# Kernel tuning notes

Hardware: AMD Instinct MI355X
Metric: run time of the kernel (lower is better)

## Reference

```python
import jax, jax.numpy as jnp
import numpy as np

B, T, D, H, G = 32, 1000, 512, 512, 8
LN_EPS = 1e-5


def setup_inputs() -> dict:
    key = jax.random.key(0)
    ks = jax.random.split(key, 6)
    return {
        "x": jax.random.normal(ks[0], (B, T, D), jnp.float32),
        "w_in": jax.random.normal(ks[1], (G, D // G, H // G), jnp.float32) * 0.05,
        "w_rec_W": jax.random.normal(ks[2], (2 * H, H), jnp.float32) * 0.05,
        "u_rec": jax.random.normal(ks[3], (2 * H, H), jnp.float32) * 0.05,
        "ln_gamma": jnp.ones((2 * H,), jnp.float32),
        "ln_beta": jnp.zeros((2 * H,), jnp.float32),
        "w_out": jax.random.normal(ks[4], (G, H // G, D // G), jnp.float32) * 0.05,
    }


def grouped_linear(x, w):
    # x: [B,T,G*I], w: [G,I,Ho] -> [B,T,G*Ho]
    b, t, _ = x.shape
    g, i, ho = w.shape
    y = jnp.einsum('btgi,gih->btgh', x.reshape(b, t, g, i), w)
    return y.reshape(b, t, g * ho)


def layernorm(w, gamma, beta):
    mu = jnp.mean(w, axis=-1, keepdims=True)
    var = jnp.var(w, axis=-1, keepdims=True)
    return (w - mu) * jax.lax.rsqrt(var + LN_EPS) * gamma + beta


def ligru_scan(w, u):
    # w: [B,T,2H] precomputed input projection; u: [2H,H] recurrent weight
    ut = u.T  # [H, 2H]
    h0 = jnp.zeros((w.shape[0], u.shape[1]), w.dtype)

    def step(h, wt):
        gates = wt + h @ ut            # [B, 2H]
        at, zt = jnp.split(gates, 2, axis=1)
        zt = jax.nn.sigmoid(zt)
        hcand = jax.nn.relu(at)        # drop_mask = 1.0 (eval)
        h = zt * h + (1.0 - zt) * hcand
        return h, h

    _, hs = jax.lax.scan(step, h0, jnp.swapaxes(w, 0, 1))  # [T,B,H]
    return jnp.swapaxes(hs, 0, 1)  # [B,T,H]


def reference(x, w_in, w_rec_W, u_rec, ln_gamma, ln_beta, w_out):
    h_in = grouped_linear(x, w_in)              # [B,T,H]
    w = jnp.einsum('bth,gh->btg', h_in, w_rec_W)  # [B,T,2H]
    w = layernorm(w, ln_gamma, ln_beta)
    h = ligru_scan(w, u_rec)                    # [B,T,H]
    return grouped_linear(h, w_out)             # [B,T,D]
```

## Files before the change

kernel.cpp:

```cpp
#include <hip/hip_runtime.h>
#include <cstddef>

#define B_SZ 32
#define T_LEN 1000
#define LN_EPS 1e-5f

typedef short bf16x8 __attribute__((ext_vector_type(8)));
typedef float f32x4 __attribute__((ext_vector_type(4)));

__device__ __forceinline__ unsigned short f2bf(float f) {
    unsigned u = __builtin_bit_cast(unsigned, f);
    u += 0x7FFFu + ((u >> 16) & 1u);
    return (unsigned short)(u >> 16);
}

__global__ __launch_bounds__(256) void k1(const float* __restrict__ x,
                                          const float* __restrict__ w_in,
                                          const float* __restrict__ w_rec,
                                          unsigned short* __restrict__ hin,
                                          unsigned short* __restrict__ wrt,
                                          unsigned int* __restrict__ hbuf) {
    __shared__ alignas(16) float xt[16][512];
    const int tid  = threadIdx.x;
    const int gidx = blockIdx.x * 256 + tid;
    const int row0 = blockIdx.x * 16;

    if (gidx < 2 * 32 * 512) hbuf[gidx] = 0u;

    if (gidx < 65536) {
        int lane = gidx & 63;
        int nt   = (gidx >> 6) & 63;
        int kt   = gidx >> 12;
        int n    = nt * 16 + (lane & 15);
        int k0   = kt * 32 + (lane >> 4) * 8;
        const float* src = w_rec + (size_t)n * 512 + k0;
        unsigned short* dst = wrt + (size_t)gidx * 8;
#pragma unroll
        for (int j = 0; j < 8; ++j) dst[j] = f2bf(src[j]);
    }

    for (int i = tid; i < 16 * 128; i += 256) {
        int rr = i >> 7, c4 = i & 127;
        ((float4*)xt[rr])[c4] =
            ((const float4*)(x + (size_t)(row0 + rr) * 512))[c4];
    }
    __syncthreads();

    for (int q = 0; q < 2; ++q) {
        const int c = tid + (q << 8);
        const int g = c >> 6, o = c & 63;
        const float* wb = w_in + (g << 12) + o;
        float wcol[64];
#pragma unroll
        for (int ii = 0; ii < 64; ++ii) wcol[ii] = wb[ii << 6];
#pragma unroll 4
        for (int rr = 0; rr < 16; ++rr) {
            float acc = 0.f;
#pragma unroll
            for (int ii = 0; ii < 64; ++ii) acc += xt[rr][(g << 6) + ii] * wcol[ii];
            hin[(size_t)(row0 + rr) * 512 + c] = f2bf(acc);
        }
    }
}

#define ALD 536
__global__ __launch_bounds__(256) void k2(const unsigned short* __restrict__ hin,
                                          const unsigned short* __restrict__ wrt,
                                          const float* __restrict__ gamma,
                                          const float* __restrict__ beta,
                                          float* __restrict__ w_pre) {
    __shared__ alignas(16) unsigned short At[32 * ALD];
    __shared__ float redS[4][32];
    __shared__ float redQ[4][32];
    __shared__ float stat[2][32];

    const int tid  = threadIdx.x;
    const int w    = tid >> 6;
    const int l    = tid & 63;
    const int kgrp = l >> 4;
    const int lc   = l & 15;
    const int row0 = blockIdx.x * 32;

    for (int sidx = tid; sidx < 2048; sidx += 256) {
        int r = sidx >> 6, sg = sidx & 63;
        *(bf16x8*)(At + r * ALD + sg * 8) =
            *(const bf16x8*)(hin + (size_t)(row0 + r) * 512 + sg * 8);
    }
    __syncthreads();

    f32x4 acc[2][16];
#pragma unroll
    for (int fr = 0; fr < 2; ++fr)
#pragma unroll
        for (int n = 0; n < 16; ++n) acc[fr][n] = f32x4{0.f, 0.f, 0.f, 0.f};

    for (int kt = 0; kt < 16; ++kt) {
        bf16x8 a0 = *(const bf16x8*)(At + (lc)      * ALD + kt * 32 + kgrp * 8);
        bf16x8 a1 = *(const bf16x8*)(At + (16 + lc) * ALD + kt * 32 + kgrp * 8);
        const unsigned short* bb =
            wrt + (((size_t)kt * 64 + w * 16) * 64 + l) * 8;
#pragma unroll
        for (int ntl = 0; ntl < 16; ++ntl) {
            bf16x8 bf = *(const bf16x8*)(bb + (size_t)ntl * 512);
            acc[0][ntl] = __builtin_amdgcn_mfma_f32_16x16x32_bf16(a0, bf, acc[0][ntl], 0, 0, 0);
            acc[1][ntl] = __builtin_amdgcn_mfma_f32_16x16x32_bf16(a1, bf, acc[1][ntl], 0, 0, 0);
        }
    }

    float sums[2][4] = {{0.f}}, sqs[2][4] = {{0.f}};
#pragma unroll
    for (int fr = 0; fr < 2; ++fr)
#pragma unroll
        for (int ntl = 0; ntl < 16; ++ntl)
#pragma unroll
            for (int r = 0; r < 4; ++r) {
                float v = acc[fr][ntl][r];
                sums[fr][r] += v;
                sqs[fr][r]  += v * v;
            }
#pragma unroll
    for (int off = 1; off < 16; off <<= 1)
#pragma unroll
        for (int fr = 0; fr < 2; ++fr)
#pragma unroll
            for (int r = 0; r < 4; ++r) {
                sums[fr][r] += __shfl_xor(sums[fr][r], off);
                sqs[fr][r]  += __shfl_xor(sqs[fr][r], off);
            }
    if (lc == 0) {
#pragma unroll
        for (int fr = 0; fr < 2; ++fr)
#pragma unroll
            for (int r = 0; r < 4; ++r) {
                redS[w][fr * 16 + kgrp * 4 + r] = sums[fr][r];
                redQ[w][fr * 16 + kgrp * 4 + r] = sqs[fr][r];
            }
    }
    __syncthreads();
    if (tid < 32) {
        float S = redS[0][tid] + redS[1][tid] + redS[2][tid] + redS[3][tid];
        float Q = redQ[0][tid] + redQ[1][tid] + redQ[2][tid] + redQ[3][tid];
        float mu  = S * (1.f / 1024.f);
        float var = Q * (1.f / 1024.f) - mu * mu;
        stat[0][tid] = mu;
        stat[1][tid] = rsqrtf(var + LN_EPS);
    }
    __syncthreads();

#pragma unroll
    for (int ntl = 0; ntl < 16; ++ntl) {
        const int col = (w << 8) + (ntl << 4) + lc;
        const float g = gamma[col], bt = beta[col];
#pragma unroll
        for (int fr = 0; fr < 2; ++fr)
#pragma unroll
            for (int r = 0; r < 4; ++r) {
                const int row = fr * 16 + kgrp * 4 + r;
                const float mu  = stat[0][row];
                const float inv = stat[1][row];
                w_pre[((size_t)(row0 + row) << 10) + col] =
                    (acc[fr][ntl][r] - mu) * inv * g + bt;
            }
    }
}

__global__ __launch_bounds__(1024) void k_scan(const float* __restrict__ w_pre,
                                               const float* __restrict__ u,
                                               float* __restrict__ hs,
                                               unsigned int* hbuf) {
    __shared__ alignas(16) float hsh[512];
    __shared__ float gsum[128];

    const int tid = threadIdx.x;
    const int b   = blockIdx.x & 31;
    const int s   = blockIdx.x >> 5;
    const int J0  = s << 6;
    const int row = tid >> 3;
    const int kk  = tid & 7;
    const int jj  = (row < 64) ? (J0 + row) : (448 + J0 + row);

    float ur[64];
    {
        const float4* up = (const float4*)(u + (size_t)jj * 512 + (kk << 6));
#pragma unroll
        for (int m = 0; m < 16; ++m) {
            float4 v = up[m];
            ur[4 * m + 0] = v.x; ur[4 * m + 1] = v.y;
            ur[4 * m + 2] = v.z; ur[4 * m + 3] = v.w;
        }
    }

    const float* wbase = w_pre + ((size_t)b * T_LEN) * 1024 + jj;
    float* outbase = hs + ((size_t)b * T_LEN) * 512 + J0;
    const char* hb8 = (const char*)hsh;

    float hreg = 0.f;
    float wcur = 0.f;
    if (kk == 0) wcur = wbase[0];

    for (int t = 0; t < T_LEN; ++t) {
        unsigned int* in_w  = hbuf + ((((t & 1) << 5) | b) << 9);
        unsigned int* out_w = hbuf + (((((t + 1) & 1) << 5) | b) << 9);

        float wnext = 0.f;
        if (kk == 0 && t + 1 < T_LEN) wnext = wbase[(size_t)(t + 1) << 10];

        if (tid < 256) {
            const unsigned long long* src = (const unsigned long long*)in_w + tid;
            const unsigned int want = (unsigned)t & 3u;
            unsigned long long v = __hip_atomic_load(src, __ATOMIC_RELAXED,
                                                     __HIP_MEMORY_SCOPE_AGENT);
            while (((unsigned)v & 3u) != want ||
                   ((unsigned)(v >> 32) & 3u) != want) {
                v = __hip_atomic_load(src, __ATOMIC_RELAXED,
                                      __HIP_MEMORY_SCOPE_AGENT);
            }
            int c = tid >> 1;
            int a = (c & ~7) | ((c ^ (c >> 4)) & 7);
            *(unsigned long long*)((char*)hsh + (a << 4) + ((tid & 1) << 3)) = v;
        }
        __syncthreads();

        float a0 = 0.f, a1 = 0.f, a2 = 0.f, a3 = 0.f;
        const int base = kk << 8;
#pragma unroll
        for (int i = 0; i < 16; ++i) {
            int off = base + (((i & 8) | ((i ^ kk) & 7)) << 4);
            float4 hv = *(const float4*)(hb8 + off);
            a0 += ur[4 * i + 0] * hv.x;
            a1 += ur[4 * i + 1] * hv.y;
            a2 += ur[4 * i + 2] * hv.z;
            a3 += ur[4 * i + 3] * hv.w;
        }
        float acc = (a0 + a1) + (a2 + a3);
        acc += __shfl_xor(acc, 1);
        acc += __shfl_xor(acc, 2);
        acc += __shfl_xor(acc, 4);
        if (kk == 0) gsum[row] = acc + wcur;
        __syncthreads();

        if (tid < 64) {
            float a  = gsum[tid];
            float zl = gsum[64 + tid];
            float z  = 1.f / (1.f + __expf(-zl));
            float hn = z * hreg + (1.f - z) * fmaxf(a, 0.f);
            hreg = hn;
            unsigned int bits = (__builtin_bit_cast(unsigned int, hn) & ~3u) |
                                ((unsigned)(t + 1) & 3u);
            __hip_atomic_store(out_w + J0 + tid, bits, __ATOMIC_RELAXED,
                               __HIP_MEMORY_SCOPE_AGENT);
            outbase[((size_t)t << 9) + tid] = hn;
        }
        wcur = wnext;
    }
}

__global__ __launch_bounds__(256) void k_out(const float* __restrict__ w_out,
                                             float* __restrict__ io) {
    __shared__ alignas(16) unsigned short At[32 * ALD];

    const int tid  = threadIdx.x;
    const int w    = tid >> 6;
    const int l    = tid & 63;
    const int kgrp = l >> 4;
    const int lc   = l & 15;
    const int row0 = blockIdx.x * 32;

    for (int sidx = tid; sidx < 2048; sidx += 256) {
        int r = sidx >> 6, c8 = sidx & 63;
        const float4* src = (const float4*)(io + (size_t)(row0 + r) * 512 + c8 * 8);
        float4 v0 = src[0], v1 = src[1];
        unsigned short tmp[8] = {f2bf(v0.x), f2bf(v0.y), f2bf(v0.z), f2bf(v0.w),
                                 f2bf(v1.x), f2bf(v1.y), f2bf(v1.z), f2bf(v1.w)};
        *(bf16x8*)(At + r * ALD + c8 * 8) = *(bf16x8*)tmp;
    }
    __syncthreads();

    bf16x8 bfr[16];
#pragma unroll
    for (int gi = 0; gi < 2; ++gi) {
        const int g = 2 * w + gi;
#pragma unroll
        for (int kt = 0; kt < 2; ++kt) {
            const float* bsrc = w_out + (g << 12) + (kt * 32 + kgrp * 8) * 64 + lc;
#pragma unroll
            for (int nt = 0; nt < 4; ++nt) {
                unsigned short bw[8];
#pragma unroll
                for (int j = 0; j < 8; ++j) bw[j] = f2bf(bsrc[j * 64 + nt * 16]);
                bfr[(gi * 2 + kt) * 4 + nt] = *(bf16x8*)bw;
            }
        }
    }

    f32x4 acc[2][8];
#pragma unroll
    for (int fr = 0; fr < 2; ++fr)
#pragma unroll
        for (int n = 0; n < 8; ++n) acc[fr][n] = f32x4{0.f, 0.f, 0.f, 0.f};

#pragma unroll
    for (int gi = 0; gi < 2; ++gi) {
        const int g = 2 * w + gi;
#pragma unroll
        for (int kt = 0; kt < 2; ++kt) {
            bf16x8 a0 = *(const bf16x8*)(At + lc        * ALD + g * 64 + kt * 32 + kgrp * 8);
            bf16x8 a1 = *(const bf16x8*)(At + (16 + lc) * ALD + g * 64 + kt * 32 + kgrp * 8);
#pragma unroll
            for (int nt = 0; nt < 4; ++nt) {
                bf16x8 bf = bfr[(gi * 2 + kt) * 4 + nt];
                acc[0][gi * 4 + nt] = __builtin_amdgcn_mfma_f32_16x16x32_bf16(a0, bf, acc[0][gi * 4 + nt], 0, 0, 0);
                acc[1][gi * 4 + nt] = __builtin_amdgcn_mfma_f32_16x16x32_bf16(a1, bf, acc[1][gi * 4 + nt], 0, 0, 0);
            }
        }
    }

#pragma unroll
    for (int gi = 0; gi < 2; ++gi)
#pragma unroll
        for (int nt = 0; nt < 4; ++nt) {
            const int col = (2 * w + gi) * 64 + nt * 16 + lc;
#pragma unroll
            for (int fr = 0; fr < 2; ++fr)
#pragma unroll
                for (int r = 0; r < 4; ++r)
                    io[(size_t)(row0 + fr * 16 + kgrp * 4 + r) * 512 + col] =
                        acc[fr][gi * 4 + nt][r];
        }
}

extern "C" void kernel_launch(void* const* d_in, const int* in_sizes, int n_in,
                              void* d_out, int out_size, void* d_ws, size_t ws_size,
                              hipStream_t stream) {
    const float* x      = (const float*)d_in[0];
    const float* w_in   = (const float*)d_in[1];
    const float* w_rec  = (const float*)d_in[2];
    const float* u_rec  = (const float*)d_in[3];
    const float* gamma  = (const float*)d_in[4];
    const float* beta   = (const float*)d_in[5];
    const float* w_out  = (const float*)d_in[6];
    float* out = (float*)d_out;

    float*        w_pre = (float*)d_ws;
    unsigned int* hbuf  = (unsigned int*)(w_pre + (size_t)32 * T_LEN * 1024);

    unsigned short* hin = (unsigned short*)d_out;
    unsigned short* wrt = hin + (size_t)32000 * 512;

    hipLaunchKernelGGL(k1, dim3(2000), dim3(256), 0, stream,
                       x, w_in, w_rec, hin, wrt, hbuf);
    hipLaunchKernelGGL(k2, dim3(1000), dim3(256), 0, stream,
                       hin, wrt, gamma, beta, w_pre);
    hipLaunchKernelGGL(k_scan, dim3(256), dim3(1024), 0, stream,
                       w_pre, u_rec, out, hbuf);
    hipLaunchKernelGGL(k_out, dim3(1000), dim3(256), 0, stream, w_out, out);
}
```

Measured before the change: 1.661 ms.

## Compute grouped input projection with bf16 MFMA instead of scalar FP32 FMAs

Rewrites k1's grouped linear so x is converted to bf16 in LDS and the product uses 16x16x32 bf16 MFMA instructions. Each block now handles 32 rows with half as many blocks, and the result is staged through LDS for coalesced 16-byte stores. This replaces a scalar FMA loop with register-held weight columns, but rounding x and w_in to bf16 adds error. Every block still converts its w_in fragments to bf16 on its own.

```diff
diff --git a/kernel.cpp b/kernel.cpp
--- a/kernel.cpp
+++ b/kernel.cpp
@@ -4,6 +4,7 @@
 #define B_SZ 32
 #define T_LEN 1000
 #define LN_EPS 1e-5f
+#define ALD 536
 
 typedef short bf16x8 __attribute__((ext_vector_type(8)));
 typedef float f32x4 __attribute__((ext_vector_type(4)));
@@ -20,10 +21,15 @@
                                           unsigned short* __restrict__ hin,
                                           unsigned short* __restrict__ wrt,
                                           unsigned int* __restrict__ hbuf) {
-    __shared__ alignas(16) float xt[16][512];
+    __shared__ alignas(16) unsigned short At[32 * ALD];
+
     const int tid  = threadIdx.x;
     const int gidx = blockIdx.x * 256 + tid;
-    const int row0 = blockIdx.x * 16;
+    const int w    = tid >> 6;
+    const int l    = tid & 63;
+    const int kgrp = l >> 4;
+    const int lc   = l & 15;
+    const int row0 = blockIdx.x * 32;
 
     if (gidx < 2 * 32 * 512) hbuf[gidx] = 0u;
 
@@ -39,31 +45,77 @@
         for (int j = 0; j < 8; ++j) dst[j] = f2bf(src[j]);
     }
 
-    for (int i = tid; i < 16 * 128; i += 256) {
-        int rr = i >> 7, c4 = i & 127;
-        ((float4*)xt[rr])[c4] =
-            ((const float4*)(x + (size_t)(row0 + rr) * 512))[c4];
-    }
-    __syncthreads();
-
-    for (int q = 0; q < 2; ++q) {
-        const int c = tid + (q << 8);
-        const int g = c >> 6, o = c & 63;
-        const float* wb = w_in + (g << 12) + o;
-        float wcol[64];
-#pragma unroll
-        for (int ii = 0; ii < 64; ++ii) wcol[ii] = wb[ii << 6];
-#pragma unroll 4
-        for (int rr = 0; rr < 16; ++rr) {
-            float acc = 0.f;
-#pragma unroll
-            for (int ii = 0; ii < 64; ++ii) acc += xt[rr][(g << 6) + ii] * wcol[ii];
-            hin[(size_t)(row0 + rr) * 512 + c] = f2bf(acc);
-        }
-    }
-}
-
-#define ALD 536
+    for (int sidx = tid; sidx < 2048; sidx += 256) {
+        int r = sidx >> 6, c8 = sidx & 63;
+        const float4* src = (const float4*)(x + (size_t)(row0 + r) * 512 + c8 * 8);
+        float4 v0 = src[0], v1 = src[1];
+        unsigned short tmp[8] = {f2bf(v0.x), f2bf(v0.y), f2bf(v0.z), f2bf(v0.w),
+                                 f2bf(v1.x), f2bf(v1.y), f2bf(v1.z), f2bf(v1.w)};
+        *(bf16x8*)(At + r * ALD + c8 * 8) = *(bf16x8*)tmp;
+    }
+    __syncthreads();
+
+    bf16x8 bfr[16];
+#pragma unroll
+    for (int gi = 0; gi < 2; ++gi) {
+        const int g = 2 * w + gi;
+#pragma unroll
+        for (int kt = 0; kt < 2; ++kt) {
+            const float* bsrc = w_in + (g << 12) + (kt * 32 + kgrp * 8) * 64 + lc;
+#pragma unroll
+            for (int nt = 0; nt < 4; ++nt) {
+                unsigned short bw[8];
+#pragma unroll
+                for (int j = 0; j < 8; ++j) bw[j] = f2bf(bsrc[j * 64 + nt * 16]);
+                bfr[(gi * 2 + kt) * 4 + nt] = *(bf16x8*)bw;
+            }
+        }
+    }
+
+    f32x4 acc[2][8];
+#pragma unroll
+    for (int fr = 0; fr < 2; ++fr)
+#pragma unroll
+        for (int n = 0; n < 8; ++n) acc[fr][n] = f32x4{0.f, 0.f, 0.f, 0.f};
+
+#pragma unroll
+    for (int gi = 0; gi < 2; ++gi) {
+        const int g = 2 * w + gi;
+#pragma unroll
+        for (int kt = 0; kt < 2; ++kt) {
+            bf16x8 a0 = *(const bf16x8*)(At + lc        * ALD + g * 64 + kt * 32 + kgrp * 8);
+            bf16x8 a1 = *(const bf16x8*)(At + (16 + lc) * ALD + g * 64 + kt * 32 + kgrp * 8);
+#pragma unroll
+            for (int nt = 0; nt < 4; ++nt) {
+                bf16x8 bf = bfr[(gi * 2 + kt) * 4 + nt];
+                acc[0][gi * 4 + nt] = __builtin_amdgcn_mfma_f32_16x16x32_bf16(a0, bf, acc[0][gi * 4 + nt], 0, 0, 0);
+                acc[1][gi * 4 + nt] = __builtin_amdgcn_mfma_f32_16x16x32_bf16(a1, bf, acc[1][gi * 4 + nt], 0, 0, 0);
+            }
+        }
+    }
+    __syncthreads();
+
+#pragma unroll
+    for (int gi = 0; gi < 2; ++gi)
+#pragma unroll
+        for (int nt = 0; nt < 4; ++nt) {
+            const int col = (2 * w + gi) * 64 + nt * 16 + lc;
+#pragma unroll
+            for (int fr = 0; fr < 2; ++fr)
+#pragma unroll
+                for (int r = 0; r < 4; ++r)
+                    At[(fr * 16 + kgrp * 4 + r) * ALD + col] =
+                        f2bf(acc[fr][gi * 4 + nt][r]);
+        }
+    __syncthreads();
+
+    for (int sidx = tid; sidx < 2048; sidx += 256) {
+        int r = sidx >> 6, c8 = sidx & 63;
+        *(bf16x8*)(hin + (size_t)(row0 + r) * 512 + c8 * 8) =
+            *(const bf16x8*)(At + r * ALD + c8 * 8);
+    }
+}
+
 __global__ __launch_bounds__(256) void k2(const unsigned short* __restrict__ hin,
                                           const unsigned short* __restrict__ wrt,
                                           const float* __restrict__ gamma,
@@ -347,7 +399,7 @@
     unsigned short* hin = (unsigned short*)d_out;
     unsigned short* wrt = hin + (size_t)32000 * 512;
 
-    hipLaunchKernelGGL(k1, dim3(2000), dim3(256), 0, stream,
+    hipLaunchKernelGGL(k1, dim3(1000), dim3(256), 0, stream,
                        x, w_in, w_rec, hin, wrt, hbuf);
     hipLaunchKernelGGL(k2, dim3(1000), dim3(256), 0, stream,
                        hin, wrt, gamma, beta, w_pre);
```

Result: faster. 1.625 ms (-2.2%).
